# Optimization experiments

Measured on AMD Instinct MI355X. Metric: run time of the kernel, lower is better.

Reference implementation:

```python
import jax, jax.numpy as jnp
import numpy as np

U = 4096        # n_users
I = 16384       # n_items
D = 64          # embed_dim
N = U + I       # interaction-graph nodes
NE_I = 524288   # interaction edges (nonzeros of norm_inter_graph)
NE_S = 65536    # social edges
L_INTER = 3     # LightGCN layers on user-item graph
L_SOC = 2       # WeightGCN layers (graph powers) on social graph
NEG_INF = jnp.float32(-1e30)


def setup_inputs() -> dict:
    key = jax.random.key(0)
    ks = jax.random.split(key, 13)
    return {
        'user_emb': jax.random.normal(ks[0], (U, D), jnp.float32) * 0.1,
        'item_emb': jax.random.normal(ks[1], (I, D), jnp.float32) * 0.1,
        'inter_vals': jax.random.uniform(ks[2], (NE_I,), jnp.float32) * 0.05,  # D^-1/2 A D^-1/2 values
        'Wa': jax.random.normal(ks[3], (D, D), jnp.float32) * 0.1,
        'Wb': jax.random.normal(ks[4], (D, D), jnp.float32) * 0.1,
        'w1': jax.random.normal(ks[5], (2 * D, D), jnp.float32) * 0.1,
        'b1': jnp.zeros((D,), jnp.float32),
        'w2': jax.random.normal(ks[6], (D, 1), jnp.float32) * 0.1,
        'b2': jnp.zeros((1,), jnp.float32),
        'inter_rows': jax.random.randint(ks[7], (NE_I,), 0, N, jnp.int32),
        'inter_cols': jax.random.randint(ks[8], (NE_I,), 0, N, jnp.int32),
        'social_rows': jax.random.randint(ks[9], (NE_S,), 0, U, jnp.int32),
        'social_cols': jax.random.randint(ks[10], (NE_S,), 0, U, jnp.int32),
    }


def _spmm(rows, cols, vals, x, n):
    # sparse [n,n] @ dense [n,d] via gather + segment_sum (torch.sparse.mm)
    return jax.ops.segment_sum(vals[:, None] * x[cols], rows, num_segments=n)


def _lightgcn(rows, cols, vals, embed, n, n_layers):
    embs = [embed]
    h = embed
    for _ in range(n_layers):
        h = _spmm(rows, cols, vals, h, n)
        embs.append(h)
    return jnp.mean(jnp.stack(embs, axis=1), axis=1)  # [n, d]


def _masked_row_softmax(g, m):
    # torch.sparse.softmax: softmax over stored (structural) entries per row
    logits = jnp.where(m, g, NEG_INF)
    s = jax.nn.softmax(logits, axis=1)
    return jnp.where(m.any(axis=1, keepdims=True), s, 0.0)


def reference(user_emb, item_emb, inter_vals, Wa, Wb, w1, b1, w2, b2,
              inter_rows, inter_cols, social_rows, social_cols):
    # ---- LightGCN on user-item interaction graph ----
    inter_emb = jnp.concatenate([user_emb, item_emb], axis=0)           # [N, D]
    inter_out = _lightgcn(inter_rows, inter_cols, inter_vals, inter_emb, N, L_INTER)
    user_e, item_e = inter_out[:U], inter_out[U:]

    # ---- edge-activation MLP (infer_activation): h = cols, t = rows ----
    feat = jnp.concatenate([user_emb[social_cols] @ Wa,
                            user_emb[social_rows] @ Wb], axis=1)        # [NE_S, 2D]
    hid = jax.nn.relu(feat @ w1 + b1)
    p = (hid @ w2 + b2)[:, 0]
    edge_w = jax.nn.sigmoid(p)                                          # [NE_S]

    # ---- weighted social graph (duplicates coalesce by sum) ----
    A = jnp.zeros((U, U), jnp.float32).at[social_rows, social_cols].add(edge_w)
    B = (A > 0).astype(jnp.float32)  # structural pattern (non-diff)

    # ---- WeightGCN: graph powers + per-row sparse softmax ----
    graphs, masks = [A], [A > 0]
    g_prev, b_prev = A, B
    for _ in range(L_SOC - 1):
        g_prev = g_prev @ A
        b_prev = b_prev @ B
        graphs.append(g_prev)
        masks.append(b_prev > 0)
    sembs = [user_e]
    for g, m in zip(graphs, masks):
        sembs.append(_masked_row_softmax(g, m) @ user_e)
    social_e2 = jnp.mean(jnp.stack(sembs, axis=1), axis=1)              # [U, D]

    # ---- final user embedding (bpr_loss path) ----
    return user_e + social_e2
```

## Files before the change

### kernel.cpp

```cpp
#include <hip/hip_runtime.h>
#include <hip/hip_bf16.h>

#define U_    4096
#define I_    16384
#define D_    64
#define N_    20480
#define NEI   524288
#define NES   65536
#define CAPI  96
#define RCAPS 64
#define SEG   384

__global__ __launch_bounds__(256) void init_wab2_kernel(int* __restrict__ cnt, int* __restrict__ skey,
                                                        float* __restrict__ sval,
                                                        const float* __restrict__ Wa,
                                                        const float* __restrict__ Wb,
                                                        const float* __restrict__ w1,
                                                        float* __restrict__ Wa2, float* __restrict__ Wb2) {
    int b = blockIdx.x;
    if (b < 1024) {
        int tid = b * 256 + threadIdx.x;
        int stride = 1024 * 256;
        for (int o = tid; o < N_; o += stride) cnt[o] = 0;
        for (int o = tid; o < U_ * RCAPS; o += stride) { skey[o] = -1; sval[o] = 0.f; }
    } else {
        int o = (b - 1024) * 256 + threadIdx.x;
        int mat = o >> 12;
        int i = (o >> 6) & 63;
        int j = o & 63;
        const float* M  = mat ? Wb : Wa;
        const float* W1 = w1 + mat * 64 * 64;
        float s = 0.f;
        #pragma unroll 8
        for (int k = 0; k < 64; ++k) s += M[i * 64 + k] * W1[k * 64 + j];
        (mat ? Wb2 : Wa2)[i * 64 + j] = s;
    }
}

__global__ void scatter_i_kernel(const int* __restrict__ rows, const int* __restrict__ cols,
                                 const float* __restrict__ vals,
                                 int* __restrict__ cnt, int2* __restrict__ ed) {
    int e = blockIdx.x * 256 + threadIdx.x;
    int r = rows[e];
    int pos = atomicAdd(&cnt[r], 1);
    if (pos < CAPI) ed[(size_t)r * CAPI + pos] = make_int2(cols[e], __float_as_int(vals[e]));
}

__global__ __launch_bounds__(256) void spmm1_pab_kernel(const int* __restrict__ cnt, const int2* __restrict__ ed,
                                                        const float* __restrict__ ue, const float* __restrict__ ie,
                                                        float* __restrict__ h1,
                                                        const float* __restrict__ Wa2, const float* __restrict__ Wb2,
                                                        float* __restrict__ Pa, float* __restrict__ Pb) {
    int b = blockIdx.x;
    int wv = threadIdx.x >> 6, lane = threadIdx.x & 63;
    if (b < 5120) {
        int w = b * 4 + wv;
        int n = cnt[w]; if (n > CAPI) n = CAPI;
        const int2* row = ed + (size_t)w * CAPI;
        float acc = 0.f;
        #pragma unroll 4
        for (int j = 0; j < n; ++j) {
            int2 e = row[j];
            int c = e.x; float v = __int_as_float(e.y);
            const float* xp = (c < U_) ? (ue + (size_t)c * D_) : (ie + (size_t)(c - U_) * D_);
            acc += v * xp[lane];
        }
        h1[(size_t)w * D_ + lane] = acc;
    } else {
        int w = (b - 5120) * 4 + wv;
        float x = ue[w * 64 + lane];
        float accA = 0.f, accB = 0.f;
        #pragma unroll 8
        for (int k = 0; k < 64; ++k) {
            float xk = __shfl(x, k);
            accA += xk * Wa2[k * 64 + lane];
            accB += xk * Wb2[k * 64 + lane];
        }
        Pa[w * 64 + lane] = accA;
        Pb[w * 64 + lane] = accB;
    }
}

__global__ __launch_bounds__(256) void spmm2_edge_kernel(const int* __restrict__ cnt, const int2* __restrict__ ed,
                                                         const float* __restrict__ x, float* __restrict__ y,
                                                         const int* __restrict__ sr, const int* __restrict__ sc,
                                                         const float* __restrict__ Pa, const float* __restrict__ Pb,
                                                         const float* __restrict__ b1, const float* __restrict__ w2,
                                                         const float* __restrict__ b2,
                                                         int* __restrict__ skey, float* __restrict__ sval) {
    int b = blockIdx.x;
    if (b < 5120) {
        int wv = threadIdx.x >> 6, lane = threadIdx.x & 63;
        int w = b * 4 + wv;
        int n = cnt[w]; if (n > CAPI) n = CAPI;
        const int2* row = ed + (size_t)w * CAPI;
        float acc = 0.f;
        #pragma unroll 4
        for (int j = 0; j < n; ++j) {
            int2 e = row[j];
            acc += __int_as_float(e.y) * x[(size_t)e.x * D_ + lane];
        }
        y[(size_t)w * D_ + lane] = acc;
    } else {
        int w = (b - 5120) * 16 + (threadIdx.x >> 4);
        int q = threadIdx.x & 15;
        int r = sr[w], c = sc[w];
        float4 pa = ((const float4*)Pa)[c * 16 + q];
        float4 pb = ((const float4*)Pb)[r * 16 + q];
        float4 bb = ((const float4*)b1)[q];
        float4 ww = ((const float4*)w2)[q];
        float hx = fmaxf(pa.x + pb.x + bb.x, 0.f);
        float hy = fmaxf(pa.y + pb.y + bb.y, 0.f);
        float hz = fmaxf(pa.z + pb.z + bb.z, 0.f);
        float hw = fmaxf(pa.w + pb.w + bb.w, 0.f);
        float t = hx * ww.x + hy * ww.y + hz * ww.z + hw * ww.w;
        t += __shfl_xor(t, 8);
        t += __shfl_xor(t, 4);
        t += __shfl_xor(t, 2);
        t += __shfl_xor(t, 1);
        if (q == 0) {
            float p = t + b2[0];
            float ew = 1.f / (1.f + expf(-p));
            size_t base = (size_t)r * RCAPS;
            int hh = c & (RCAPS - 1);
            for (int probe = 0; probe < RCAPS; ++probe) {
                int prev = atomicCAS(&skey[base + hh], -1, c);
                if (prev == -1 || prev == c) { atomicAdd(&sval[base + hh], ew); break; }
                hh = (hh + 1) & (RCAPS - 1);
            }
        }
    }
}

__global__ __launch_bounds__(256) void spmm_last_kernel(const int* __restrict__ cnt, const int2* __restrict__ ed,
                                                        const float* __restrict__ ue,
                                                        const float* __restrict__ h1, const float* __restrict__ h2,
                                                        float* __restrict__ user_e) {
    int w = (blockIdx.x * 256 + threadIdx.x) >> 6;
    int lane = threadIdx.x & 63;
    int n = cnt[w]; if (n > CAPI) n = CAPI;
    const int2* row = ed + (size_t)w * CAPI;
    float acc = 0.f;
    #pragma unroll 4
    for (int j = 0; j < n; ++j) {
        int2 e = row[j];
        acc += __int_as_float(e.y) * h2[(size_t)e.x * D_ + lane];
    }
    size_t o = (size_t)w * D_ + lane;
    user_e[o] = 0.25f * (ue[o] + h1[o] + h2[o] + acc);
}


__device__ __forceinline__ float wave_max_(float v) {
    #pragma unroll
    for (int o = 32; o > 0; o >>= 1) v = fmaxf(v, __shfl_xor(v, o));
    return v;
}
__device__ __forceinline__ float wave_sum_(float v) {
    #pragma unroll
    for (int o = 32; o > 0; o >>= 1) v += __shfl_xor(v, o);
    return v;
}

__global__ __launch_bounds__(256) void social_kernel(const int* __restrict__ skey,
                                                     const float* __restrict__ sval,
                                                     const float* __restrict__ user_e,
                                                     float* __restrict__ out) {
    __shared__ float row2[U_];
    __shared__ int   list2[4][SEG];
    __shared__ float val2[4][SEG];
    __shared__ int   kcol_s[RCAPS];
    __shared__ float kval_s[RCAPS];
    __shared__ float wredm[4], wreds[4];
    __shared__ float accw[4][64];
    __shared__ int   cntw[4];
    __shared__ int   nnz_s;

    int i = blockIdx.x, t = threadIdx.x;
    int wv = t >> 6, lane = t & 63;

    {
        float4* r4 = (float4*)row2;
        #pragma unroll
        for (int u = 0; u < 4; ++u) r4[t + 256 * u] = make_float4(0.f, 0.f, 0.f, 0.f);
    }
    if (t < 4) cntw[t] = 0;

    if (wv == 0) {
        int k = skey[(size_t)i * RCAPS + lane];
        float v = sval[(size_t)i * RCAPS + lane];
        unsigned long long mask = __ballot(k >= 0);
        int pos = __popcll(mask & ((1ull << lane) - 1ull));
        if (k >= 0) { kcol_s[pos] = k; kval_s[pos] = v; }
        if (lane == 0) nnz_s = __popcll(mask);
    }
    __syncthreads();
    int nnz = nnz_s;

    float kv  = (lane < nnz) ? kval_s[lane] : -1e30f;
    float m1  = wave_max_(kv);
    float ex  = (lane < nnz) ? expf(kv - m1) : 0.f;
    float S1  = wave_sum_(ex);
    float inv1 = (nnz > 0) ? 1.f / S1 : 0.f;

    for (int e = wv; e < nnz; e += 4) {
        int k = kcol_s[e];
        float vk = kval_s[e];
        int   c2 = skey[(size_t)k * RCAPS + lane];
        float v2 = sval[(size_t)k * RCAPS + lane];
        if (c2 >= 0) {
            float old = atomicAdd(&row2[c2], vk * v2);
            if (old == 0.f) {
                int idx = atomicAdd(&cntw[wv], 1);
                if (idx < SEG) list2[wv][idx] = c2;
            }
        }
    }

    float acc = 0.f;
    for (int e = wv; e < nnz; e += 4) {
        float p = __shfl(ex, e) * inv1;
        acc += p * user_e[(size_t)kcol_s[e] * D_ + lane];
    }
    __syncthreads();

    int len[4];
    #pragma unroll
    for (int s = 0; s < 4; ++s) { int L = cntw[s]; len[s] = (L > SEG) ? SEG : L; }
    int cnt2 = len[0] + len[1] + len[2] + len[3];

    float lm = -1e30f;
    #pragma unroll
    for (int s = 0; s < 4; ++s)
        for (int e = t; e < len[s]; e += 256) lm = fmaxf(lm, row2[list2[s][e]]);
    lm = wave_max_(lm);
    if (lane == 0) wredm[wv] = lm;
    __syncthreads();
    float m2 = fmaxf(fmaxf(wredm[0], wredm[1]), fmaxf(wredm[2], wredm[3]));
    float ls = 0.f;
    #pragma unroll
    for (int s = 0; s < 4; ++s)
        for (int e = t; e < len[s]; e += 256) {
            float exv = expf(row2[list2[s][e]] - m2);
            val2[s][e] = exv;
            ls += exv;
        }
    ls = wave_sum_(ls);
    if (lane == 0) wreds[wv] = ls;
    __syncthreads();
    float S2 = wreds[0] + wreds[1] + wreds[2] + wreds[3];
    float inv2 = (cnt2 > 0) ? 1.f / S2 : 0.f;

    #pragma unroll
    for (int s = 0; s < 4; ++s) {
        #pragma unroll 4
        for (int e = wv; e < len[s]; e += 4) {
            acc += (val2[s][e] * inv2) * user_e[(size_t)list2[s][e] * D_ + lane];
        }
    }
    accw[wv][lane] = acc;
    __syncthreads();
    if (t < 64) {
        float s = accw[0][t] + accw[1][t] + accw[2][t] + accw[3][t];
        float ue = user_e[(size_t)i * D_ + t];
        out[i * D_ + t] = (4.f * ue + s) * (1.f / 3.f);
    }
}


extern "C" void kernel_launch(void* const* d_in, const int* in_sizes, int n_in,
                              void* d_out, int out_size, void* d_ws, size_t ws_size,
                              hipStream_t stream) {
    (void)in_sizes; (void)n_in; (void)out_size; (void)ws_size;
    const float* user_emb  = (const float*)d_in[0];
    const float* item_emb  = (const float*)d_in[1];
    const float* inter_vals= (const float*)d_in[2];
    const float* Wa        = (const float*)d_in[3];
    const float* Wb        = (const float*)d_in[4];
    const float* w1        = (const float*)d_in[5];
    const float* b1        = (const float*)d_in[6];
    const float* w2        = (const float*)d_in[7];
    const float* b2        = (const float*)d_in[8];
    const int* inter_rows  = (const int*)d_in[9];
    const int* inter_cols  = (const int*)d_in[10];
    const int* social_rows = (const int*)d_in[11];
    const int* social_cols = (const int*)d_in[12];
    float* out = (float*)d_out;

    char* w = (char*)d_ws;
    auto alloc = [&](size_t bytes) -> void* {
        void* p = (void*)w;
        w += (bytes + 255) & ~(size_t)255;
        return p;
    };
    float* h1     = (float*)alloc((size_t)N_ * D_ * 4);
    float* h2     = (float*)alloc((size_t)N_ * D_ * 4);
    float* user_e = (float*)alloc((size_t)U_ * D_ * 4);
    float* Pa     = (float*)alloc((size_t)U_ * D_ * 4);
    float* Pb     = (float*)alloc((size_t)U_ * D_ * 4);
    float* Wa2    = (float*)alloc(64 * 64 * 4);
    float* Wb2    = (float*)alloc(64 * 64 * 4);
    int*   cnt    = (int*)alloc((size_t)N_ * 4);
    int2*  ed     = (int2*)alloc((size_t)N_ * CAPI * 8);
    int*   skey   = (int*)alloc((size_t)U_ * RCAPS * 4);
    float* sval   = (float*)alloc((size_t)U_ * RCAPS * 4);

    init_wab2_kernel<<<1056, 256, 0, stream>>>(cnt, skey, sval, Wa, Wb, w1, Wa2, Wb2);
    scatter_i_kernel<<<NEI / 256, 256, 0, stream>>>(inter_rows, inter_cols, inter_vals, cnt, ed);
    spmm1_pab_kernel<<<6144, 256, 0, stream>>>(cnt, ed, user_emb, item_emb, h1, Wa2, Wb2, Pa, Pb);
    spmm2_edge_kernel<<<9216, 256, 0, stream>>>(cnt, ed, h1, h2, social_rows, social_cols,
                                                Pa, Pb, b1, w2, b2, skey, sval);
    spmm_last_kernel<<<1024, 256, 0, stream>>>(cnt, ed, user_emb, h1, h2, user_e);
    social_kernel<<<U_, 256, 0, stream>>>(skey, sval, user_e, out);
}
```

Before: 226.2 us.

## Store LightGCN embeddings in bf16 and widen social kernel to 8 waves

```diff
diff --git a/kernel.cpp b/kernel.cpp
--- a/kernel.cpp
+++ b/kernel.cpp
@@ -9,10 +9,16 @@
 #define NES   65536
 #define CAPI  96
 #define RCAPS 64
-#define SEG   384
+#define NW    8
+#define SEG   192
+
+typedef __hip_bfloat16 bf16;
 
 __global__ __launch_bounds__(256) void init_wab2_kernel(int* __restrict__ cnt, int* __restrict__ skey,
                                                         float* __restrict__ sval,
+                                                        const float* __restrict__ ue,
+                                                        const float* __restrict__ ie,
+                                                        bf16* __restrict__ xb,
                                                         const float* __restrict__ Wa,
                                                         const float* __restrict__ Wb,
                                                         const float* __restrict__ w1,
@@ -23,6 +29,10 @@
         int stride = 1024 * 256;
         for (int o = tid; o < N_; o += stride) cnt[o] = 0;
         for (int o = tid; o < U_ * RCAPS; o += stride) { skey[o] = -1; sval[o] = 0.f; }
+        for (int o = tid; o < N_ * D_; o += stride) {
+            float v = (o < U_ * D_) ? ue[o] : ie[o - U_ * D_];
+            xb[o] = __float2bfloat16(v);
+        }
     } else {
         int o = (b - 1024) * 256 + threadIdx.x;
         int mat = o >> 12;
@@ -47,8 +57,9 @@
 }
 
 __global__ __launch_bounds__(256) void spmm1_pab_kernel(const int* __restrict__ cnt, const int2* __restrict__ ed,
-                                                        const float* __restrict__ ue, const float* __restrict__ ie,
-                                                        float* __restrict__ h1,
+                                                        const bf16* __restrict__ xb,
+                                                        const float* __restrict__ ue,
+                                                        bf16* __restrict__ h1b,
                                                         const float* __restrict__ Wa2, const float* __restrict__ Wb2,
                                                         float* __restrict__ Pa, float* __restrict__ Pb) {
     int b = blockIdx.x;
@@ -61,11 +72,9 @@
         #pragma unroll 4
         for (int j = 0; j < n; ++j) {
             int2 e = row[j];
-            int c = e.x; float v = __int_as_float(e.y);
-            const float* xp = (c < U_) ? (ue + (size_t)c * D_) : (ie + (size_t)(c - U_) * D_);
-            acc += v * xp[lane];
-        }
-        h1[(size_t)w * D_ + lane] = acc;
+            acc += __int_as_float(e.y) * __bfloat162float(xb[(size_t)e.x * D_ + lane]);
+        }
+        h1b[(size_t)w * D_ + lane] = __float2bfloat16(acc);
     } else {
         int w = (b - 5120) * 4 + wv;
         float x = ue[w * 64 + lane];
@@ -82,7 +91,7 @@
 }
 
 __global__ __launch_bounds__(256) void spmm2_edge_kernel(const int* __restrict__ cnt, const int2* __restrict__ ed,
-                                                         const float* __restrict__ x, float* __restrict__ y,
+                                                         const bf16* __restrict__ h1b, bf16* __restrict__ h2b,
                                                          const int* __restrict__ sr, const int* __restrict__ sc,
                                                          const float* __restrict__ Pa, const float* __restrict__ Pb,
                                                          const float* __restrict__ b1, const float* __restrict__ w2,
@@ -98,9 +107,9 @@
         #pragma unroll 4
         for (int j = 0; j < n; ++j) {
             int2 e = row[j];
-            acc += __int_as_float(e.y) * x[(size_t)e.x * D_ + lane];
-        }
-        y[(size_t)w * D_ + lane] = acc;
+            acc += __int_as_float(e.y) * __bfloat162float(h1b[(size_t)e.x * D_ + lane]);
+        }
+        h2b[(size_t)w * D_ + lane] = __float2bfloat16(acc);
     } else {
         int w = (b - 5120) * 16 + (threadIdx.x >> 4);
         int q = threadIdx.x & 15;
@@ -134,7 +143,7 @@
 
 __global__ __launch_bounds__(256) void spmm_last_kernel(const int* __restrict__ cnt, const int2* __restrict__ ed,
                                                         const float* __restrict__ ue,
-                                                        const float* __restrict__ h1, const float* __restrict__ h2,
+                                                        const bf16* __restrict__ h1b, const bf16* __restrict__ h2b,
                                                         float* __restrict__ user_e) {
     int w = (blockIdx.x * 256 + threadIdx.x) >> 6;
     int lane = threadIdx.x & 63;
@@ -144,10 +153,10 @@
     #pragma unroll 4
     for (int j = 0; j < n; ++j) {
         int2 e = row[j];
-        acc += __int_as_float(e.y) * h2[(size_t)e.x * D_ + lane];
+        acc += __int_as_float(e.y) * __bfloat162float(h2b[(size_t)e.x * D_ + lane]);
     }
     size_t o = (size_t)w * D_ + lane;
-    user_e[o] = 0.25f * (ue[o] + h1[o] + h2[o] + acc);
+    user_e[o] = 0.25f * (ue[o] + __bfloat162float(h1b[o]) + __bfloat162float(h2b[o]) + acc);
 }
 
 
@@ -162,18 +171,18 @@
     return v;
 }
 
-__global__ __launch_bounds__(256) void social_kernel(const int* __restrict__ skey,
+__global__ __launch_bounds__(512) void social_kernel(const int* __restrict__ skey,
                                                      const float* __restrict__ sval,
                                                      const float* __restrict__ user_e,
                                                      float* __restrict__ out) {
     __shared__ float row2[U_];
-    __shared__ int   list2[4][SEG];
-    __shared__ float val2[4][SEG];
+    __shared__ int   list2[NW][SEG];
+    __shared__ float val2[NW][SEG];
     __shared__ int   kcol_s[RCAPS];
     __shared__ float kval_s[RCAPS];
-    __shared__ float wredm[4], wreds[4];
-    __shared__ float accw[4][64];
-    __shared__ int   cntw[4];
+    __shared__ float wredm[NW], wreds[NW];
+    __shared__ float accw[NW][64];
+    __shared__ int   cntw[NW];
     __shared__ int   nnz_s;
 
     int i = blockIdx.x, t = threadIdx.x;
@@ -181,10 +190,10 @@
 
     {
         float4* r4 = (float4*)row2;
-        #pragma unroll
-        for (int u = 0; u < 4; ++u) r4[t + 256 * u] = make_float4(0.f, 0.f, 0.f, 0.f);
-    }
-    if (t < 4) cntw[t] = 0;
+        r4[t] = make_float4(0.f, 0.f, 0.f, 0.f);
+        r4[t + 512] = make_float4(0.f, 0.f, 0.f, 0.f);
+    }
+    if (t < NW) cntw[t] = 0;
 
     if (wv == 0) {
         int k = skey[(size_t)i * RCAPS + lane];
@@ -203,7 +212,7 @@
     float S1  = wave_sum_(ex);
     float inv1 = (nnz > 0) ? 1.f / S1 : 0.f;
 
-    for (int e = wv; e < nnz; e += 4) {
+    for (int e = wv; e < nnz; e += NW) {
         int k = kcol_s[e];
         float vk = kval_s[e];
         int   c2 = skey[(size_t)k * RCAPS + lane];
@@ -218,50 +227,56 @@
     }
 
     float acc = 0.f;
-    for (int e = wv; e < nnz; e += 4) {
+    for (int e = wv; e < nnz; e += NW) {
         float p = __shfl(ex, e) * inv1;
         acc += p * user_e[(size_t)kcol_s[e] * D_ + lane];
     }
     __syncthreads();
 
-    int len[4];
-    #pragma unroll
-    for (int s = 0; s < 4; ++s) { int L = cntw[s]; len[s] = (L > SEG) ? SEG : L; }
-    int cnt2 = len[0] + len[1] + len[2] + len[3];
+    int mylen = cntw[wv]; if (mylen > SEG) mylen = SEG;
+    int cnt2 = 0;
+    #pragma unroll
+    for (int s = 0; s < NW; ++s) { int L = cntw[s]; cnt2 += (L > SEG) ? SEG : L; }
 
     float lm = -1e30f;
-    #pragma unroll
-    for (int s = 0; s < 4; ++s)
-        for (int e = t; e < len[s]; e += 256) lm = fmaxf(lm, row2[list2[s][e]]);
+    for (int e = lane; e < mylen; e += 64) {
+        float v = row2[list2[wv][e]];
+        val2[wv][e] = v;
+        lm = fmaxf(lm, v);
+    }
     lm = wave_max_(lm);
     if (lane == 0) wredm[wv] = lm;
     __syncthreads();
-    float m2 = fmaxf(fmaxf(wredm[0], wredm[1]), fmaxf(wredm[2], wredm[3]));
+    float m2 = -1e30f;
+    #pragma unroll
+    for (int s = 0; s < NW; ++s) m2 = fmaxf(m2, wredm[s]);
     float ls = 0.f;
-    #pragma unroll
-    for (int s = 0; s < 4; ++s)
-        for (int e = t; e < len[s]; e += 256) {
-            float exv = expf(row2[list2[s][e]] - m2);
-            val2[s][e] = exv;
-            ls += exv;
-        }
+    for (int e = lane; e < mylen; e += 64) {
+        float exv = expf(val2[wv][e] - m2);
+        val2[wv][e] = exv;
+        ls += exv;
+    }
     ls = wave_sum_(ls);
     if (lane == 0) wreds[wv] = ls;
     __syncthreads();
-    float S2 = wreds[0] + wreds[1] + wreds[2] + wreds[3];
+    float S2 = 0.f;
+    #pragma unroll
+    for (int s = 0; s < NW; ++s) S2 += wreds[s];
     float inv2 = (cnt2 > 0) ? 1.f / S2 : 0.f;
 
     #pragma unroll
-    for (int s = 0; s < 4; ++s) {
-        #pragma unroll 4
-        for (int e = wv; e < len[s]; e += 4) {
+    for (int s = 0; s < NW; ++s) {
+        int L = cntw[s]; if (L > SEG) L = SEG;
+        for (int e = wv; e < L; e += NW) {
             acc += (val2[s][e] * inv2) * user_e[(size_t)list2[s][e] * D_ + lane];
         }
     }
     accw[wv][lane] = acc;
     __syncthreads();
     if (t < 64) {
-        float s = accw[0][t] + accw[1][t] + accw[2][t] + accw[3][t];
+        float s = accw[0][t];
+        #pragma unroll
+        for (int s2 = 1; s2 < NW; ++s2) s += accw[s2][t];
         float ue = user_e[(size_t)i * D_ + t];
         out[i * D_ + t] = (4.f * ue + s) * (1.f / 3.f);
     }
@@ -293,8 +308,9 @@
         w += (bytes + 255) & ~(size_t)255;
         return p;
     };
-    float* h1     = (float*)alloc((size_t)N_ * D_ * 4);
-    float* h2     = (float*)alloc((size_t)N_ * D_ * 4);
+    bf16*  xb     = (bf16*)alloc((size_t)N_ * D_ * 2);
+    bf16*  h1b    = (bf16*)alloc((size_t)N_ * D_ * 2);
+    bf16*  h2b    = (bf16*)alloc((size_t)N_ * D_ * 2);
     float* user_e = (float*)alloc((size_t)U_ * D_ * 4);
     float* Pa     = (float*)alloc((size_t)U_ * D_ * 4);
     float* Pb     = (float*)alloc((size_t)U_ * D_ * 4);
@@ -305,11 +321,12 @@
     int*   skey   = (int*)alloc((size_t)U_ * RCAPS * 4);
     float* sval   = (float*)alloc((size_t)U_ * RCAPS * 4);
 
-    init_wab2_kernel<<<1056, 256, 0, stream>>>(cnt, skey, sval, Wa, Wb, w1, Wa2, Wb2);
+    init_wab2_kernel<<<1056, 256, 0, stream>>>(cnt, skey, sval, user_emb, item_emb, xb,
+                                               Wa, Wb, w1, Wa2, Wb2);
     scatter_i_kernel<<<NEI / 256, 256, 0, stream>>>(inter_rows, inter_cols, inter_vals, cnt, ed);
-    spmm1_pab_kernel<<<6144, 256, 0, stream>>>(cnt, ed, user_emb, item_emb, h1, Wa2, Wb2, Pa, Pb);
-    spmm2_edge_kernel<<<9216, 256, 0, stream>>>(cnt, ed, h1, h2, social_rows, social_cols,
+    spmm1_pab_kernel<<<6144, 256, 0, stream>>>(cnt, ed, xb, user_emb, h1b, Wa2, Wb2, Pa, Pb);
+    spmm2_edge_kernel<<<9216, 256, 0, stream>>>(cnt, ed, h1b, h2b, social_rows, social_cols,
                                                 Pa, Pb, b1, w2, b2, skey, sval);
-    spmm_last_kernel<<<1024, 256, 0, stream>>>(cnt, ed, user_emb, h1, h2, user_e);
-    social_kernel<<<U_, 256, 0, stream>>>(skey, sval, user_e, out);
-}
+    spmm_last_kernel<<<1024, 256, 0, stream>>>(cnt, ed, user_emb, h1b, h2b, user_e);
+    social_kernel<<<U_, 512, 0, stream>>>(skey, sval, user_e, out);
+}
```

After: 229.3 us. No clear change (+1.4%).
